# Performance work log

Hardware: AMD Instinct MI355X
Metric: run time of the kernel (lower is better)

## Reference

```python
import jax, jax.numpy as jnp
import numpy as np

N = 8192          # number of nodes
DIN = 512         # in_features
DOUT = 256        # out_features
P_EDGE = 0.004    # ~32 avg degree
NEG_INF = -9e15   # matches the torch module's -9000000000000000.0 mask value


def setup_inputs() -> dict:
    key = jax.random.key(0)
    ks = jax.random.split(key, 7)
    x = jax.random.normal(ks[0], (N, DIN), dtype=jnp.float32)
    # binary adjacency, Bernoulli(P_EDGE)
    adj = (jax.random.uniform(ks[1], (N, N)) < P_EDGE).astype(jnp.float32)
    W1 = jax.random.normal(ks[2], (DIN, DOUT), dtype=jnp.float32) * 0.05
    b1 = jnp.zeros((DOUT,), dtype=jnp.float32)
    a1_w = jax.random.normal(ks[3], (DOUT,), dtype=jnp.float32) * 0.05
    a1_b = jnp.zeros((), dtype=jnp.float32)
    a2_w = jax.random.normal(ks[4], (DOUT,), dtype=jnp.float32) * 0.05
    a2_b = jnp.zeros((), dtype=jnp.float32)
    return {"x": x, "adj": adj, "W1": W1, "b1": b1,
            "a1_w": a1_w, "a1_b": a1_b, "a2_w": a2_w, "a2_b": a2_b}


def reference(x, adj, W1, b1, a1_w, a1_b, a2_w, a2_b):
    # h = linear1(elu(x))                       [n, DOUT]
    h = jnp.matmul(jax.nn.elu(x), W1) + b1
    # per-node scalar scores g1 (source/col) and g2 (dest/row)
    g1 = h @ a1_w + a1_b                       # [n]
    g2 = h @ a2_w + a2_b                       # [n]
    # kron trick collapses to: scores[i,j] = adj[i,j] * (g2[i] + g1[j])
    scores = adj * (g2[:, None] + g1[None, :])  # [n, n]
    e = jax.nn.leaky_relu(scores, negative_slope=0.2)
    attention = jax.nn.softmax(jnp.where(adj > 0, e, NEG_INF), axis=1)
    # untied=False path: weighted aggregation of h (dropout p=0 is identity)
    return attention @ h
```

## Files before the change

### kernel.cpp

```cpp
#include <hip/hip_runtime.h>
#include <hip/hip_bf16.h>
#include <cstdint>
#include <cstddef>

#define N_NODES 8192
#define DIN 512
#define DOUT 256
#define CAP 512

typedef short bf16x8 __attribute__((ext_vector_type(8)));
typedef float f32x4 __attribute__((ext_vector_type(4)));
typedef unsigned int u32x4 __attribute__((ext_vector_type(4)));

__device__ __forceinline__ float bf2f(unsigned short u) {
    union { unsigned int ui; float f; } v; v.ui = ((unsigned int)u) << 16; return v.f;
}
__device__ __forceinline__ unsigned short f2bf(float f) {
    union { float f; unsigned int u; } v; v.f = f;
    unsigned int u = v.u;
    return (unsigned short)((u + 0x7fffu + ((u >> 16) & 1u)) >> 16);
}
__device__ __forceinline__ float elu1(float v) { return v > 0.f ? v : (expf(v) - 1.f); }

__global__ __launch_bounds__(256) void convw_kernel(
    const float* __restrict__ W1, unsigned short* __restrict__ wb)
{
    const int n = blockIdx.x;
    const int k = threadIdx.x * 2;
    unsigned short a = f2bf(W1[(size_t)k * DOUT + n]);
    unsigned short b = f2bf(W1[(size_t)(k + 1) * DOUT + n]);
    *(unsigned int*)(wb + (size_t)n * DIN + k) = (unsigned int)a | ((unsigned int)b << 16);
}

__global__ __launch_bounds__(256) void gemm_h_kernel(
    const float* __restrict__ x, const unsigned short* __restrict__ wb,
    const float* __restrict__ b1, unsigned short* __restrict__ h)
{
    const int tid = threadIdx.x;
    const int wave = tid >> 6, lane = tid & 63;
    const int quad = lane >> 4, r16 = lane & 15;
    const int m0 = blockIdx.x * 16;
    const int n0 = wave * 64;

    f32x4 acc[4] = {{0.f,0.f,0.f,0.f},{0.f,0.f,0.f,0.f},{0.f,0.f,0.f,0.f},{0.f,0.f,0.f,0.f}};
    const float* xrow = x + (size_t)(m0 + r16) * DIN;

    for (int k0 = 0; k0 < DIN; k0 += 32) {
        const int kb = k0 + quad * 8;
        float4 f0 = *(const float4*)(xrow + kb);
        float4 f1 = *(const float4*)(xrow + kb + 4);
        bf16x8 A;
        A[0] = (short)f2bf(elu1(f0.x)); A[1] = (short)f2bf(elu1(f0.y));
        A[2] = (short)f2bf(elu1(f0.z)); A[3] = (short)f2bf(elu1(f0.w));
        A[4] = (short)f2bf(elu1(f1.x)); A[5] = (short)f2bf(elu1(f1.y));
        A[6] = (short)f2bf(elu1(f1.z)); A[7] = (short)f2bf(elu1(f1.w));
        bf16x8 B[4];
        #pragma unroll
        for (int s = 0; s < 4; ++s)
            B[s] = *(const bf16x8*)(wb + (size_t)(n0 + s * 16 + r16) * DIN + kb);
        #pragma unroll
        for (int ni = 0; ni < 4; ++ni)
            acc[ni] = __builtin_amdgcn_mfma_f32_16x16x32_bf16(A, B[ni], acc[ni], 0, 0, 0);
    }
    #pragma unroll
    for (int ni = 0; ni < 4; ++ni) {
        const int col = n0 + ni * 16 + r16;
        const float bias = b1[col];
        #pragma unroll
        for (int rr = 0; rr < 4; ++rr)
            h[(size_t)(m0 + quad * 4 + rr) * DOUT + col] = f2bf(acc[ni][rr] + bias);
    }
}

__global__ __launch_bounds__(256) void g12_kernel(
    const unsigned short* __restrict__ h,
    const float* __restrict__ a1w, const float* __restrict__ a1b,
    const float* __restrict__ a2w, const float* __restrict__ a2b,
    float* __restrict__ g1, float* __restrict__ g2)
{
    const int tid = threadIdx.x;
    const int wave = tid >> 6, lane = tid & 63;
    const int i = blockIdx.x * 4 + wave;
    const int d0 = lane * 4;
    ushort4 hv = *(const ushort4*)(h + (size_t)i * DOUT + d0);
    float4 w1 = *(const float4*)(a1w + d0);
    float4 w2 = *(const float4*)(a2w + d0);
    float h0 = bf2f(hv.x), h1 = bf2f(hv.y), h2 = bf2f(hv.z), h3 = bf2f(hv.w);
    float s1 = h0*w1.x + h1*w1.y + h2*w1.z + h3*w1.w;
    float s2 = h0*w2.x + h1*w2.y + h2*w2.z + h3*w2.w;
    #pragma unroll
    for (int off = 32; off > 0; off >>= 1) {
        s1 += __shfl_xor(s1, off, 64);
        s2 += __shfl_xor(s2, off, 64);
    }
    if (lane == 0) {
        g1[i] = s1 + a1b[0];
        g2[i] = s2 + a2b[0];
    }
}

__global__ __launch_bounds__(256) void agg_kernel(
    const float* __restrict__ adj, const unsigned short* __restrict__ h,
    const float* __restrict__ g1, const float* __restrict__ g2,
    float* __restrict__ out)
{
    __shared__ int   eidx[CAP];
    __shared__ float ev[CAP];
    __shared__ float red[256];
    __shared__ int   cnt;

    const int tid = threadIdx.x;
    const int i = blockIdx.x;
    if (tid == 0) cnt = 0;
    __syncthreads();

    const float g2i = g2[i];
    const float* arow = adj + (size_t)i * N_NODES;

    u32x4 raws[8];
    #pragma unroll
    for (int c = 0; c < 8; ++c)
        raws[c] = __builtin_nontemporal_load((const u32x4*)(arow + c * 1024 + tid * 4));

    #pragma unroll
    for (int c = 0; c < 8; ++c) {
        u32x4 raw = raws[c];
        if (raw.x | raw.y | raw.z | raw.w) {
            unsigned int wv[4] = {raw.x, raw.y, raw.z, raw.w};
            #pragma unroll
            for (int q = 0; q < 4; ++q) {
                if (wv[q]) {
                    int j = c * 1024 + tid * 4 + q;
                    union { unsigned int u; float f; } av; av.u = wv[q];
                    float s = av.f * (g2i + g1[j]);
                    float lr = s > 0.f ? s : 0.2f * s;
                    int pos = atomicAdd(&cnt, 1);
                    if (pos < CAP) { eidx[pos] = j; ev[pos] = lr; }
                }
            }
        }
    }
    __syncthreads();
    const int K = cnt < CAP ? cnt : CAP;

    if (K == 0) {
        float acc = 0.f;
        for (int j = 0; j < N_NODES; ++j) acc += bf2f(h[(size_t)j * DOUT + tid]);
        out[(size_t)i * DOUT + tid] = acc / (float)N_NODES;
        return;
    }

    float mloc = -1e30f;
    for (int k = tid; k < K; k += 256) mloc = fmaxf(mloc, ev[k]);
    red[tid] = mloc; __syncthreads();
    for (int s = 128; s > 0; s >>= 1) {
        if (tid < s) red[tid] = fmaxf(red[tid], red[tid + s]);
        __syncthreads();
    }
    const float m = red[0];
    __syncthreads();

    float sloc = 0.f;
    for (int k = tid; k < K; k += 256) { float p = expf(ev[k] - m); ev[k] = p; sloc += p; }
    red[tid] = sloc; __syncthreads();
    for (int s = 128; s > 0; s >>= 1) {
        if (tid < s) red[tid] += red[tid + s];
        __syncthreads();
    }
    const float inv = 1.f / red[0];

    float acc = 0.f;
    int k = 0;
    for (; k + 4 <= K; k += 4) {
        float p0 = ev[k],     p1 = ev[k + 1], p2 = ev[k + 2], p3 = ev[k + 3];
        int   j0 = eidx[k],   j1 = eidx[k+1], j2 = eidx[k+2], j3 = eidx[k+3];
        float v0 = bf2f(h[(size_t)j0 * DOUT + tid]);
        float v1 = bf2f(h[(size_t)j1 * DOUT + tid]);
        float v2 = bf2f(h[(size_t)j2 * DOUT + tid]);
        float v3 = bf2f(h[(size_t)j3 * DOUT + tid]);
        acc += p0 * v0 + p1 * v1 + p2 * v2 + p3 * v3;
    }
    for (; k < K; ++k) acc += ev[k] * bf2f(h[(size_t)eidx[k] * DOUT + tid]);
    out[(size_t)i * DOUT + tid] = acc * inv;
}

extern "C" void kernel_launch(void* const* d_in, const int* in_sizes, int n_in,
                              void* d_out, int out_size, void* d_ws, size_t ws_size,
                              hipStream_t stream) {
    const float* x   = (const float*)d_in[0];
    const float* adj = (const float*)d_in[1];
    const float* W1  = (const float*)d_in[2];
    const float* b1  = (const float*)d_in[3];
    const float* a1w = (const float*)d_in[4];
    const float* a1b = (const float*)d_in[5];
    const float* a2w = (const float*)d_in[6];
    const float* a2b = (const float*)d_in[7];

    char* w = (char*)d_ws;
    float* g1 = (float*)w;                     w += (size_t)N_NODES * 4;
    float* g2 = (float*)w;                     w += (size_t)N_NODES * 4;
    unsigned short* h  = (unsigned short*)w;   w += (size_t)N_NODES * DOUT * 2;
    unsigned short* wb = (unsigned short*)w;
    float* out = (float*)d_out;

    hipLaunchKernelGGL(convw_kernel,  dim3(256),  dim3(256), 0, stream, W1, wb);
    hipLaunchKernelGGL(gemm_h_kernel, dim3(512),  dim3(256), 0, stream, x, wb, b1, h);
    hipLaunchKernelGGL(g12_kernel,    dim3(2048), dim3(256), 0, stream, h, a1w, a1b, a2w, a2b, g1, g2);
    hipLaunchKernelGGL(agg_kernel,    dim3(8192), dim3(256), 0, stream, adj, h, g1, g2, out);
}
```

Before: 404.0 us.

## Precompress adjacency into a nibble bitmask in a separate streaming pass

A new mask_kernel streams the dense fp32 adjacency once and packs it into a compact bitmask of 4 bits per byte. The aggregation kernel then reads that bitmask instead of the dense row. The goal is to keep the large streaming read in a simple bandwidth-bound kernel, apart from the latency-bound gather and softmax work. The cost is an extra launch plus writing and re-reading a small mask buffer. It also drops the multiply by the adjacency value, which is only correct because the adjacency is binary.

Result: slower. 429.9 us (+6.4%).

```diff
diff --git a/kernel.cpp b/kernel.cpp
--- a/kernel.cpp
+++ b/kernel.cpp
@@ -99,8 +99,29 @@
     }
 }
 
-__global__ __launch_bounds__(256) void agg_kernel(
-    const float* __restrict__ adj, const unsigned short* __restrict__ h,
+__global__ __launch_bounds__(256) void mask_kernel(
+    const u32x4* __restrict__ adj4, unsigned char* __restrict__ msk)
+{
+    const int gw = (blockIdx.x * 256 + threadIdx.x) >> 6;
+    const int lane = threadIdx.x & 63;
+    const size_t rowchunk = (size_t)gw * 2048;
+
+    for (int b = 0; b < 32; b += 8) {
+        u32x4 r[8];
+        #pragma unroll
+        for (int s = 0; s < 8; ++s)
+            r[s] = __builtin_nontemporal_load(&adj4[rowchunk + (size_t)(b + s) * 64 + lane]);
+        #pragma unroll
+        for (int s = 0; s < 8; ++s) {
+            unsigned char byt = (unsigned char)((r[s].x ? 1 : 0) | (r[s].y ? 2 : 0) |
+                                                (r[s].z ? 4 : 0) | (r[s].w ? 8 : 0));
+            msk[rowchunk + (size_t)(b + s) * 64 + lane] = byt;
+        }
+    }
+}
+
+__global__ __launch_bounds__(256) void finish2_kernel(
+    const unsigned char* __restrict__ msk, const unsigned short* __restrict__ h,
     const float* __restrict__ g1, const float* __restrict__ g2,
     float* __restrict__ out)
 {
@@ -115,27 +136,27 @@
     __syncthreads();
 
     const float g2i = g2[i];
-    const float* arow = adj + (size_t)i * N_NODES;
-
-    u32x4 raws[8];
+    uint2 mb = *(const uint2*)(msk + (size_t)i * 2048 + tid * 8);
+    unsigned int words[2] = {mb.x, mb.y};
     #pragma unroll
-    for (int c = 0; c < 8; ++c)
-        raws[c] = __builtin_nontemporal_load((const u32x4*)(arow + c * 1024 + tid * 4));
-
-    #pragma unroll
-    for (int c = 0; c < 8; ++c) {
-        u32x4 raw = raws[c];
-        if (raw.x | raw.y | raw.z | raw.w) {
-            unsigned int wv[4] = {raw.x, raw.y, raw.z, raw.w};
+    for (int wq = 0; wq < 2; ++wq) {
+        unsigned int wv = words[wq];
+        if (wv) {
             #pragma unroll
-            for (int q = 0; q < 4; ++q) {
-                if (wv[q]) {
-                    int j = c * 1024 + tid * 4 + q;
-                    union { unsigned int u; float f; } av; av.u = wv[q];
-                    float s = av.f * (g2i + g1[j]);
-                    float lr = s > 0.f ? s : 0.2f * s;
-                    int pos = atomicAdd(&cnt, 1);
-                    if (pos < CAP) { eidx[pos] = j; ev[pos] = lr; }
+            for (int u = 0; u < 4; ++u) {
+                unsigned int byt = (wv >> (u * 8)) & 0xFu;
+                if (byt) {
+                    const int colbase = tid * 32 + (wq * 4 + u) * 4;
+                    #pragma unroll
+                    for (int bit = 0; bit < 4; ++bit) {
+                        if (byt & (1u << bit)) {
+                            int j = colbase + bit;
+                            float s = g2i + g1[j];
+                            float lr = s > 0.f ? s : 0.2f * s;
+                            int pos = atomicAdd(&cnt, 1);
+                            if (pos < CAP) { eidx[pos] = j; ev[pos] = lr; }
+                        }
+                    }
                 }
             }
         }
@@ -200,11 +221,13 @@
     float* g1 = (float*)w;                     w += (size_t)N_NODES * 4;
     float* g2 = (float*)w;                     w += (size_t)N_NODES * 4;
     unsigned short* h  = (unsigned short*)w;   w += (size_t)N_NODES * DOUT * 2;
-    unsigned short* wb = (unsigned short*)w;
+    unsigned short* wb = (unsigned short*)w;   w += (size_t)DOUT * DIN * 2;
+    unsigned char* msk = (unsigned char*)w;
     float* out = (float*)d_out;
 
+    hipLaunchKernelGGL(mask_kernel,   dim3(2048), dim3(256), 0, stream, (const u32x4*)adj, msk);
     hipLaunchKernelGGL(convw_kernel,  dim3(256),  dim3(256), 0, stream, W1, wb);
     hipLaunchKernelGGL(gemm_h_kernel, dim3(512),  dim3(256), 0, stream, x, wb, b1, h);
     hipLaunchKernelGGL(g12_kernel,    dim3(2048), dim3(256), 0, stream, h, a1w, a1b, a2w, a2b, g1, g2);
-    hipLaunchKernelGGL(agg_kernel,    dim3(8192), dim3(256), 0, stream, adj, h, g1, g2, out);
-}
+    hipLaunchKernelGGL(finish2_kernel,dim3(8192), dim3(256), 0, stream, msk, h, g1, g2, out);
+}
```

## Compute attention scores from x directly and overlap GEMM with adjacency scan

Applied to the files above, without the earlier changes.

Attention scalars g1/g2 are now computed algebraically from elu(x)·(W1·a) instead of from h, which removes the dependency of the adjacency scan on the GEMM output. The GEMM and the per-row softmax/edge-list construction are merged into one launch so the memory-bound 256MB adjacency read can run alongside the MFMA GEMM. The softmax-weighted gather is split into a separate kernel that reads the edge lists back from global memory. This adds extra launches and the global round-trip of index/probability lists, and g1/g2 are now computed in fp32 from x rather than from bf16-rounded h, which changes rounding slightly.

After: 434.6 us. +7.6%, slower.

```diff
diff --git a/kernel.cpp b/kernel.cpp
--- a/kernel.cpp
+++ b/kernel.cpp
@@ -7,6 +7,7 @@
 #define DIN 512
 #define DOUT 256
 #define CAP 512
+#define GEMM_BLOCKS 512
 
 typedef short bf16x8 __attribute__((ext_vector_type(8)));
 typedef float f32x4 __attribute__((ext_vector_type(4)));
@@ -21,6 +22,35 @@
     return (unsigned short)((u + 0x7fffu + ((u >> 16) & 1u)) >> 16);
 }
 __device__ __forceinline__ float elu1(float v) { return v > 0.f ? v : (expf(v) - 1.f); }
+
+__global__ __launch_bounds__(256) void u12_kernel(
+    const float* __restrict__ W1,
+    const float* __restrict__ b1,
+    const float* __restrict__ a1w, const float* __restrict__ a1b,
+    const float* __restrict__ a2w, const float* __restrict__ a2b,
+    float* __restrict__ u1, float* __restrict__ u2, float* __restrict__ cc)
+{
+    const int tid = threadIdx.x;
+    if (blockIdx.x < 2) {
+        const float* av = (blockIdx.x == 0) ? a1w : a2w;
+        float* uv = (blockIdx.x == 0) ? u1 : u2;
+        for (int k = tid; k < DIN; k += 256) {
+            const float* wrow = W1 + (size_t)k * DOUT;
+            float s = 0.f;
+            for (int n = 0; n < DOUT; ++n) s += wrow[n] * av[n];
+            uv[k] = s;
+        }
+    } else {
+        __shared__ float red[256];
+        red[tid] = b1[tid] * a1w[tid]; __syncthreads();
+        for (int s = 128; s > 0; s >>= 1) { if (tid < s) red[tid] += red[tid + s]; __syncthreads(); }
+        if (tid == 0) cc[0] = red[0] + a1b[0];
+        __syncthreads();
+        red[tid] = b1[tid] * a2w[tid]; __syncthreads();
+        for (int s = 128; s > 0; s >>= 1) { if (tid < s) red[tid] += red[tid + s]; __syncthreads(); }
+        if (tid == 0) cc[1] = red[0] + a2b[0];
+    }
+}
 
 __global__ __launch_bounds__(256) void convw_kernel(
     const float* __restrict__ W1, unsigned short* __restrict__ wb)
@@ -32,85 +62,87 @@
     *(unsigned int*)(wb + (size_t)n * DIN + k) = (unsigned int)a | ((unsigned int)b << 16);
 }
 
-__global__ __launch_bounds__(256) void gemm_h_kernel(
-    const float* __restrict__ x, const unsigned short* __restrict__ wb,
-    const float* __restrict__ b1, unsigned short* __restrict__ h)
-{
-    const int tid = threadIdx.x;
-    const int wave = tid >> 6, lane = tid & 63;
-    const int quad = lane >> 4, r16 = lane & 15;
-    const int m0 = blockIdx.x * 16;
-    const int n0 = wave * 64;
-
-    f32x4 acc[4] = {{0.f,0.f,0.f,0.f},{0.f,0.f,0.f,0.f},{0.f,0.f,0.f,0.f},{0.f,0.f,0.f,0.f}};
-    const float* xrow = x + (size_t)(m0 + r16) * DIN;
-
-    for (int k0 = 0; k0 < DIN; k0 += 32) {
-        const int kb = k0 + quad * 8;
-        float4 f0 = *(const float4*)(xrow + kb);
-        float4 f1 = *(const float4*)(xrow + kb + 4);
-        bf16x8 A;
-        A[0] = (short)f2bf(elu1(f0.x)); A[1] = (short)f2bf(elu1(f0.y));
-        A[2] = (short)f2bf(elu1(f0.z)); A[3] = (short)f2bf(elu1(f0.w));
-        A[4] = (short)f2bf(elu1(f1.x)); A[5] = (short)f2bf(elu1(f1.y));
-        A[6] = (short)f2bf(elu1(f1.z)); A[7] = (short)f2bf(elu1(f1.w));
-        bf16x8 B[4];
-        #pragma unroll
-        for (int s = 0; s < 4; ++s)
-            B[s] = *(const bf16x8*)(wb + (size_t)(n0 + s * 16 + r16) * DIN + kb);
-        #pragma unroll
-        for (int ni = 0; ni < 4; ++ni)
-            acc[ni] = __builtin_amdgcn_mfma_f32_16x16x32_bf16(A, B[ni], acc[ni], 0, 0, 0);
-    }
-    #pragma unroll
-    for (int ni = 0; ni < 4; ++ni) {
-        const int col = n0 + ni * 16 + r16;
-        const float bias = b1[col];
-        #pragma unroll
-        for (int rr = 0; rr < 4; ++rr)
-            h[(size_t)(m0 + quad * 4 + rr) * DOUT + col] = f2bf(acc[ni][rr] + bias);
-    }
-}
-
-__global__ __launch_bounds__(256) void g12_kernel(
-    const unsigned short* __restrict__ h,
-    const float* __restrict__ a1w, const float* __restrict__ a1b,
-    const float* __restrict__ a2w, const float* __restrict__ a2b,
+__global__ __launch_bounds__(256) void g12x_kernel(
+    const float* __restrict__ x,
+    const float* __restrict__ u1, const float* __restrict__ u2,
+    const float* __restrict__ cc,
     float* __restrict__ g1, float* __restrict__ g2)
 {
     const int tid = threadIdx.x;
     const int wave = tid >> 6, lane = tid & 63;
     const int i = blockIdx.x * 4 + wave;
-    const int d0 = lane * 4;
-    ushort4 hv = *(const ushort4*)(h + (size_t)i * DOUT + d0);
-    float4 w1 = *(const float4*)(a1w + d0);
-    float4 w2 = *(const float4*)(a2w + d0);
-    float h0 = bf2f(hv.x), h1 = bf2f(hv.y), h2 = bf2f(hv.z), h3 = bf2f(hv.w);
-    float s1 = h0*w1.x + h1*w1.y + h2*w1.z + h3*w1.w;
-    float s2 = h0*w2.x + h1*w2.y + h2*w2.z + h3*w2.w;
+    const int k0 = lane * 8;
+    const float* xr = x + (size_t)i * DIN + k0;
+    float4 f0 = *(const float4*)xr;
+    float4 f1 = *(const float4*)(xr + 4);
+    float4 p0 = *(const float4*)(u1 + k0);
+    float4 p1 = *(const float4*)(u1 + k0 + 4);
+    float4 q0 = *(const float4*)(u2 + k0);
+    float4 q1 = *(const float4*)(u2 + k0 + 4);
+    float e0 = elu1(f0.x), e1 = elu1(f0.y), e2 = elu1(f0.z), e3 = elu1(f0.w);
+    float e4 = elu1(f1.x), e5 = elu1(f1.y), e6 = elu1(f1.z), e7 = elu1(f1.w);
+    float s1 = e0*p0.x + e1*p0.y + e2*p0.z + e3*p0.w + e4*p1.x + e5*p1.y + e6*p1.z + e7*p1.w;
+    float s2 = e0*q0.x + e1*q0.y + e2*q0.z + e3*q0.w + e4*q1.x + e5*q1.y + e6*q1.z + e7*q1.w;
     #pragma unroll
     for (int off = 32; off > 0; off >>= 1) {
         s1 += __shfl_xor(s1, off, 64);
         s2 += __shfl_xor(s2, off, 64);
     }
     if (lane == 0) {
-        g1[i] = s1 + a1b[0];
-        g2[i] = s2 + a2b[0];
-    }
-}
-
-__global__ __launch_bounds__(256) void agg_kernel(
-    const float* __restrict__ adj, const unsigned short* __restrict__ h,
+        g1[i] = s1 + cc[0];
+        g2[i] = s2 + cc[1];
+    }
+}
+
+__global__ __launch_bounds__(256) void fat_kernel(
+    const float* __restrict__ x, const unsigned short* __restrict__ wb,
+    const float* __restrict__ b1, unsigned short* __restrict__ h,
+    const float* __restrict__ adj,
     const float* __restrict__ g1, const float* __restrict__ g2,
-    float* __restrict__ out)
-{
+    int* __restrict__ jl, float* __restrict__ pl, int* __restrict__ cnts)
+{
+    const int tid = threadIdx.x;
+    if (blockIdx.x < GEMM_BLOCKS) {
+        const int wave = tid >> 6, lane = tid & 63;
+        const int quad = lane >> 4, r16 = lane & 15;
+        const int m0 = blockIdx.x * 16;
+        const int n0 = wave * 64;
+        f32x4 acc[4] = {{0.f,0.f,0.f,0.f},{0.f,0.f,0.f,0.f},{0.f,0.f,0.f,0.f},{0.f,0.f,0.f,0.f}};
+        const float* xrow = x + (size_t)(m0 + r16) * DIN;
+        for (int k0 = 0; k0 < DIN; k0 += 32) {
+            const int kb = k0 + quad * 8;
+            float4 f0 = *(const float4*)(xrow + kb);
+            float4 f1 = *(const float4*)(xrow + kb + 4);
+            bf16x8 A;
+            A[0] = (short)f2bf(elu1(f0.x)); A[1] = (short)f2bf(elu1(f0.y));
+            A[2] = (short)f2bf(elu1(f0.z)); A[3] = (short)f2bf(elu1(f0.w));
+            A[4] = (short)f2bf(elu1(f1.x)); A[5] = (short)f2bf(elu1(f1.y));
+            A[6] = (short)f2bf(elu1(f1.z)); A[7] = (short)f2bf(elu1(f1.w));
+            bf16x8 B[4];
+            #pragma unroll
+            for (int s = 0; s < 4; ++s)
+                B[s] = *(const bf16x8*)(wb + (size_t)(n0 + s * 16 + r16) * DIN + kb);
+            #pragma unroll
+            for (int ni = 0; ni < 4; ++ni)
+                acc[ni] = __builtin_amdgcn_mfma_f32_16x16x32_bf16(A, B[ni], acc[ni], 0, 0, 0);
+        }
+        #pragma unroll
+        for (int ni = 0; ni < 4; ++ni) {
+            const int col = n0 + ni * 16 + r16;
+            const float bias = b1[col];
+            #pragma unroll
+            for (int rr = 0; rr < 4; ++rr)
+                h[(size_t)(m0 + quad * 4 + rr) * DOUT + col] = f2bf(acc[ni][rr] + bias);
+        }
+        return;
+    }
+
     __shared__ int   eidx[CAP];
     __shared__ float ev[CAP];
     __shared__ float red[256];
     __shared__ int   cnt;
 
-    const int tid = threadIdx.x;
-    const int i = blockIdx.x;
+    const int i = blockIdx.x - GEMM_BLOCKS;
     if (tid == 0) cnt = 0;
     __syncthreads();
 
@@ -142,13 +174,8 @@
     }
     __syncthreads();
     const int K = cnt < CAP ? cnt : CAP;
-
-    if (K == 0) {
-        float acc = 0.f;
-        for (int j = 0; j < N_NODES; ++j) acc += bf2f(h[(size_t)j * DOUT + tid]);
-        out[(size_t)i * DOUT + tid] = acc / (float)N_NODES;
-        return;
-    }
+    if (tid == 0) cnts[i] = K;
+    if (K == 0) return;
 
     float mloc = -1e30f;
     for (int k = tid; k < K; k += 256) mloc = fmaxf(mloc, ev[k]);
@@ -169,19 +196,50 @@
     }
     const float inv = 1.f / red[0];
 
+    for (int k = tid; k < K; k += 256) {
+        jl[(size_t)i * CAP + k] = eidx[k];
+        pl[(size_t)i * CAP + k] = ev[k] * inv;
+    }
+}
+
+__global__ __launch_bounds__(256) void gather_kernel(
+    const int* __restrict__ jl, const float* __restrict__ pl,
+    const int* __restrict__ cnts, const unsigned short* __restrict__ h,
+    float* __restrict__ out)
+{
+    __shared__ int   jbuf[CAP];
+    __shared__ float pbuf[CAP];
+
+    const int tid = threadIdx.x;
+    const int i = blockIdx.x;
+    int K = cnts[i]; if (K > CAP) K = CAP;
+
+    if (K == 0) {
+        float acc = 0.f;
+        for (int j = 0; j < N_NODES; ++j) acc += bf2f(h[(size_t)j * DOUT + tid]);
+        out[(size_t)i * DOUT + tid] = acc / (float)N_NODES;
+        return;
+    }
+
+    for (int k = tid; k < K; k += 256) {
+        jbuf[k] = jl[(size_t)i * CAP + k];
+        pbuf[k] = pl[(size_t)i * CAP + k];
+    }
+    __syncthreads();
+
     float acc = 0.f;
     int k = 0;
     for (; k + 4 <= K; k += 4) {
-        float p0 = ev[k],     p1 = ev[k + 1], p2 = ev[k + 2], p3 = ev[k + 3];
-        int   j0 = eidx[k],   j1 = eidx[k+1], j2 = eidx[k+2], j3 = eidx[k+3];
+        float p0 = pbuf[k],   p1 = pbuf[k+1], p2 = pbuf[k+2], p3 = pbuf[k+3];
+        int   j0 = jbuf[k],   j1 = jbuf[k+1], j2 = jbuf[k+2], j3 = jbuf[k+3];
         float v0 = bf2f(h[(size_t)j0 * DOUT + tid]);
         float v1 = bf2f(h[(size_t)j1 * DOUT + tid]);
         float v2 = bf2f(h[(size_t)j2 * DOUT + tid]);
         float v3 = bf2f(h[(size_t)j3 * DOUT + tid]);
         acc += p0 * v0 + p1 * v1 + p2 * v2 + p3 * v3;
     }
-    for (; k < K; ++k) acc += ev[k] * bf2f(h[(size_t)eidx[k] * DOUT + tid]);
-    out[(size_t)i * DOUT + tid] = acc * inv;
+    for (; k < K; ++k) acc += pbuf[k] * bf2f(h[(size_t)jbuf[k] * DOUT + tid]);
+    out[(size_t)i * DOUT + tid] = acc;
 }
 
 extern "C" void kernel_launch(void* const* d_in, const int* in_sizes, int n_in,
@@ -199,12 +257,20 @@
     char* w = (char*)d_ws;
     float* g1 = (float*)w;                     w += (size_t)N_NODES * 4;
     float* g2 = (float*)w;                     w += (size_t)N_NODES * 4;
+    float* u1 = (float*)w;                     w += (size_t)DIN * 4;
+    float* u2 = (float*)w;                     w += (size_t)DIN * 4;
+    float* cc = (float*)w;                     w += 64;
     unsigned short* h  = (unsigned short*)w;   w += (size_t)N_NODES * DOUT * 2;
-    unsigned short* wb = (unsigned short*)w;
+    unsigned short* wb = (unsigned short*)w;   w += (size_t)DOUT * DIN * 2;
+    int* jl = (int*)w;                         w += (size_t)N_NODES * CAP * 4;
+    float* pl = (float*)w;                     w += (size_t)N_NODES * CAP * 4;
+    int* cnts = (int*)w;
     float* out = (float*)d_out;
 
+    hipLaunchKernelGGL(u12_kernel,    dim3(3),    dim3(256), 0, stream, W1, b1, a1w, a1b, a2w, a2b, u1, u2, cc);
     hipLaunchKernelGGL(convw_kernel,  dim3(256),  dim3(256), 0, stream, W1, wb);
-    hipLaunchKernelGGL(gemm_h_kernel, dim3(512),  dim3(256), 0, stream, x, wb, b1, h);
-    hipLaunchKernelGGL(g12_kernel,    dim3(2048), dim3(256), 0, stream, h, a1w, a1b, a2w, a2b, g1, g2);
-    hipLaunchKernelGGL(agg_kernel,    dim3(8192), dim3(256), 0, stream, adj, h, g1, g2, out);
-}
+    hipLaunchKernelGGL(g12x_kernel,   dim3(2048), dim3(256), 0, stream, x, u1, u2, cc, g1, g2);
+    hipLaunchKernelGGL(fat_kernel,    dim3(GEMM_BLOCKS + N_NODES), dim3(256), 0, stream,
+                       x, wb, b1, h, adj, g1, g2, jl, pl, cnts);
+    hipLaunchKernelGGL(gather_kernel, dim3(N_NODES), dim3(256), 0, stream, jl, pl, cnts, h, out);
+}
```
